# Optimization experiments

Hardware: AMD Instinct MI355X
Metric: run time of the kernel (lower is better)

Reference implementation:

```python
import jax, jax.numpy as jnp
import numpy as np
import math

B, S, D, E, H = 8, 384, 768, 768, 12
HD = E // H
MAXL = 512

def _xavier(key, shape):
    fan_in, fan_out = shape[1], shape[0]
    lim = math.sqrt(6.0 / (fan_in + fan_out))
    return jax.random.uniform(key, shape, jnp.float32, -lim, lim)

def setup_inputs() -> dict:
    key = jax.random.key(0)
    ks = jax.random.split(key, 12)
    return {
        "x": jax.random.normal(ks[0], (B, S, D), jnp.float32),
        "mask": jnp.ones((B, S), jnp.int32),
        "segment_ids": jax.random.randint(ks[1], (B, S), 0, 2).astype(jnp.int32),
        "sep_distances": jax.random.normal(ks[2], (B, S), jnp.float32),
        "Wq": _xavier(ks[3], (E, D)), "bq": jnp.zeros((E,), jnp.float32),
        "Wk": _xavier(ks[4], (E, D)), "bk": jnp.zeros((E,), jnp.float32),
        "Wv": _xavier(ks[5], (E, D)), "bv": jnp.zeros((E,), jnp.float32),
        "rel_emb": jax.random.normal(ks[6], (2 * MAXL - 1, D), jnp.float32),
        "Wpk": _xavier(ks[7], (E, D)), "bpk": jnp.zeros((E,), jnp.float32),
        "Wpq": _xavier(ks[8], (E, D)), "bpq": jnp.zeros((E,), jnp.float32),
        "same_bias": jnp.zeros((H,), jnp.float32),
        "cross_bias": jnp.zeros((H,), jnp.float32),
        "sep_scale": jnp.full((H,), 0.25, jnp.float32),
        "sep_decay": jnp.full((H,), 0.35, jnp.float32),
        "Wo": _xavier(ks[9], (D, E)), "bo": jnp.zeros((D,), jnp.float32),
    }

def reference(x, mask, segment_ids, sep_distances, Wq, bq, Wk, bk, Wv, bv,
              rel_emb, Wpk, bpk, Wpq, bpq, same_bias, cross_bias,
              sep_scale, sep_decay, Wo, bo):
    b, s, _ = x.shape
    def shape_heads(t):  # [b,s,E] -> [b,H,s,HD]
        return t.reshape(b, s, H, HD).transpose(0, 2, 1, 3)
    q = shape_heads(x @ Wq.T + bq)
    k = shape_heads(x @ Wk.T + bk)
    v = shape_heads(x @ Wv.T + bv)
    # relative positions i - j, clamped and shifted
    rel_pos = jnp.arange(s)[:, None] - jnp.arange(s)[None, :]
    rel_pos = jnp.clip(rel_pos, -(MAXL - 1), MAXL - 1) + (MAXL - 1)
    rel = rel_emb[rel_pos]                     # [s,s,D]
    pos_k = (rel @ Wpk.T + bpk).reshape(s, s, H, HD)  # [i,j,h,d]
    pos_q = (rel @ Wpq.T + bpq).reshape(s, s, H, HD)
    c2c = jnp.einsum('bhid,bhjd->bhij', q, k)
    c2p = jnp.einsum('bhid,ijhd->bhij', q, pos_k)
    p2c = jnp.einsum('ijhd,bhjd->bhij', pos_q, k)
    logits = (c2c + c2p + p2c) / math.sqrt(HD * 3.0)
    # segment bias
    same = (segment_ids[:, :, None] == segment_ids[:, None, :]).astype(jnp.float32)[:, None]  # [b,1,s,s]
    cross = 1.0 - same
    hb = lambda p: p[None, :, None, None]
    seg_bias = same * hb(same_bias) + cross * hb(cross_bias)
    abs_sep = jnp.abs(sep_distances)
    gap = jnp.abs(abs_sep[:, :, None] - abs_sep[:, None, :])[:, None]  # [b,1,s,s]
    decay = jax.nn.softplus(sep_decay)[None, :, None, None] + 1e-4
    seg_bias = seg_bias + cross * jnp.exp(-gap * decay) * hb(sep_scale)
    logits = logits + seg_bias
    # mask: [b,s] -> [b,1,1,s]
    m = mask[:, None, None, :]
    logits = jnp.where(m == 0, jnp.float32(-9e15), logits)
    attn = jax.nn.softmax(logits, axis=-1)
    vals = jnp.einsum('bhij,bhjd->bhid', attn, v)
    vals = vals.transpose(0, 2, 1, 3).reshape(b, s, E)
    return vals @ Wo.T + bo
```

## Files before the change

kernel.cpp:

```cpp
#include <hip/hip_runtime.h>
#include <math.h>

#define B_  8
#define S_  384
#define H_  12
#define HD_ 64
#define E_  768
#define D_  768

typedef float  floatx4 __attribute__((ext_vector_type(4)));
typedef __bf16 bf16x8  __attribute__((ext_vector_type(8)));
typedef unsigned int ux4 __attribute__((ext_vector_type(4)));

__device__ __forceinline__ unsigned short f2bf(float f) {
    union { float f; unsigned u; } x; x.f = f;
    unsigned r = x.u + 0x7fff + ((x.u >> 16) & 1);
    return (unsigned short)(r >> 16);
}
__device__ __forceinline__ float bf2f(unsigned short u) {
    union { unsigned u; float f; } x; x.u = ((unsigned)u) << 16;
    return x.f;
}
__device__ __forceinline__ bf16x8 gld8(const unsigned short* p) {
    return __builtin_bit_cast(bf16x8, *(const ux4*)p);
}
__device__ __forceinline__ int tadr(int row, int cD) {
    return (row * 8 + (cD ^ (row & 7))) * 8;
}
__device__ __forceinline__ bf16x8 lds8(const unsigned short* base, int row, int cD) {
    return __builtin_bit_cast(bf16x8, *(const ux4*)(base + tadr(row, cD)));
}

__global__ __launch_bounds__(256) void convert_all(
    const float* __restrict__ x,
    const float* __restrict__ Wq, const float* __restrict__ Wk,
    const float* __restrict__ Wv, const float* __restrict__ Wo,
    const float* __restrict__ Wpk, const float* __restrict__ Wpq,
    const float* __restrict__ rel128,
    unsigned short* __restrict__ xb,
    unsigned short* __restrict__ wqb, unsigned short* __restrict__ wkb,
    unsigned short* __restrict__ wvb, unsigned short* __restrict__ wob,
    unsigned short* __restrict__ wpkb, unsigned short* __restrict__ wpqb,
    unsigned short* __restrict__ relb)
{
    const int seg = blockIdx.y;
    const int e = (blockIdx.x * 256 + threadIdx.x) * 4;
    const float* src;
    unsigned short* dst;
    if (seg < 4)       { src = x + (size_t)seg * 589824; dst = xb + (size_t)seg * 589824; }
    else if (seg == 4) { src = Wq;  dst = wqb; }
    else if (seg == 5) { src = Wk;  dst = wkb; }
    else if (seg == 6) { src = Wv;  dst = wvb; }
    else if (seg == 7) { src = Wo;  dst = wob; }
    else if (seg == 8) { src = Wpk; dst = wpkb; }
    else if (seg == 9) { src = Wpq; dst = wpqb; }
    else               { src = rel128; dst = relb; }

    float4 v;
    if (seg == 10 && e >= 767 * 768) v = make_float4(0.f, 0.f, 0.f, 0.f);
    else                             v = *(const float4*)(src + e);
    ushort4 o;
    o.x = f2bf(v.x); o.y = f2bf(v.y); o.z = f2bf(v.z); o.w = f2bf(v.w);
    *(ushort4*)(dst + e) = o;
}

__global__ __launch_bounds__(256) void proj_all(
    const unsigned short* __restrict__ xb, const unsigned short* __restrict__ relb,
    const unsigned short* __restrict__ wq, const unsigned short* __restrict__ wk,
    const unsigned short* __restrict__ wv, const unsigned short* __restrict__ wpk,
    const unsigned short* __restrict__ wpq,
    const float* __restrict__ bq, const float* __restrict__ bk,
    const float* __restrict__ bv, const float* __restrict__ bpk,
    const float* __restrict__ bpq,
    unsigned short* __restrict__ qb, unsigned short* __restrict__ kb,
    unsigned short* __restrict__ vtb, unsigned short* __restrict__ pkb,
    unsigned short* __restrict__ pqb)
{
    const int bid = blockIdx.x;
    int z, mt, nt;
    if (bid < 864) {
        z = bid / 288; const int r = bid - z * 288; mt = r / 6; nt = r - mt * 6;
    } else {
        const int r2 = bid - 864; z = 3 + r2 / 72;
        const int r = r2 % 72; mt = r / 6; nt = r - mt * 6;
    }
    const int m0 = mt * 64, n0 = nt * 128;

    const unsigned short* A = (z < 3) ? xb : relb;
    const unsigned short* W = (z == 0) ? wq : (z == 1) ? wk : (z == 2) ? wv
                            : (z == 3) ? wpk : wpq;
    const float* bias = (z == 0) ? bq : (z == 1) ? bk : (z == 2) ? bv
                      : (z == 3) ? bpk : bpq;
    unsigned short* C = (z == 0) ? qb : (z == 1) ? kb : (z == 2) ? vtb
                      : (z == 3) ? pkb : pqb;

    __shared__ unsigned short As[64 * 64];
    __shared__ unsigned short Ws[128 * 64];

    const int tid  = threadIdx.x;
    const int lane = tid & 63;
    const int wv_  = tid >> 6;
    const int quad = lane >> 4, l16 = lane & 15;

    floatx4 acc[4][2];
#pragma unroll
    for (int i = 0; i < 4; ++i)
#pragma unroll
        for (int j = 0; j < 2; ++j) acc[i][j] = (floatx4){0.f, 0.f, 0.f, 0.f};

    for (int k0 = 0; k0 < 768; k0 += 64) {
        __syncthreads();
#pragma unroll
        for (int r = 0; r < 2; ++r) {
            const int idx = tid + 256 * r;
            const int row = idx >> 3, cL = idx & 7, cD = cL ^ (row & 7);
            __builtin_amdgcn_global_load_lds(
                (__attribute__((address_space(1))) void*)(A + (size_t)(m0 + row) * 768 + k0 + cD * 8),
                (__attribute__((address_space(3))) void*)&As[idx * 8], 16, 0, 0);
        }
#pragma unroll
        for (int r = 0; r < 4; ++r) {
            const int idx = tid + 256 * r;
            const int row = idx >> 3, cL = idx & 7, cD = cL ^ (row & 7);
            __builtin_amdgcn_global_load_lds(
                (__attribute__((address_space(1))) void*)(W + (size_t)(n0 + row) * 768 + k0 + cD * 8),
                (__attribute__((address_space(3))) void*)&Ws[idx * 8], 16, 0, 0);
        }
        __syncthreads();

        bf16x8 a[4][2], b[2][2];
#pragma unroll
        for (int mi = 0; mi < 4; ++mi)
#pragma unroll
            for (int kc = 0; kc < 2; ++kc)
                a[mi][kc] = lds8(As, mi * 16 + l16, kc * 4 + quad);
#pragma unroll
        for (int ni = 0; ni < 2; ++ni)
#pragma unroll
            for (int kc = 0; kc < 2; ++kc)
                b[ni][kc] = lds8(Ws, wv_ * 32 + ni * 16 + l16, kc * 4 + quad);
#pragma unroll
        for (int mi = 0; mi < 4; ++mi)
#pragma unroll
            for (int ni = 0; ni < 2; ++ni)
#pragma unroll
                for (int kc = 0; kc < 2; ++kc)
                    acc[mi][ni] = __builtin_amdgcn_mfma_f32_16x16x32_bf16(
                        a[mi][kc], b[ni][kc], acc[mi][ni], 0, 0, 0);
    }

#pragma unroll
    for (int ni = 0; ni < 2; ++ni) {
        const int n = n0 + wv_ * 32 + ni * 16 + l16;
        const float bn = bias[n];
#pragma unroll
        for (int mi = 0; mi < 4; ++mi) {
            const int mbase = m0 + mi * 16 + quad * 4;
            if (z == 2) {
                const int bb = mbase / S_, s = mbase - bb * S_;
                const int h = n >> 6, hd = n & 63;
                ushort4 o;
                o.x = f2bf(acc[mi][ni][0] + bn);
                o.y = f2bf(acc[mi][ni][1] + bn);
                o.z = f2bf(acc[mi][ni][2] + bn);
                o.w = f2bf(acc[mi][ni][3] + bn);
                *(ushort4*)&C[(((size_t)(bb * H_ + h) << 6) + hd) * S_ + s] = o;
            } else if (z < 2) {
#pragma unroll
                for (int reg = 0; reg < 4; ++reg) {
                    const int m = mbase + reg;
                    const int bb = m / S_, s = m - bb * S_;
                    const int h = n >> 6, hd = n & 63;
                    C[(((size_t)(bb * H_ + h) * S_ + s) << 6) + hd] =
                        f2bf(acc[mi][ni][reg] + bn);
                }
            } else {
#pragma unroll
                for (int reg = 0; reg < 4; ++reg)
                    C[(size_t)(mbase + reg) * 768 + n] = f2bf(acc[mi][ni][reg] + bn);
            }
        }
    }
}

__global__ __launch_bounds__(256) void gemm_out(
    const unsigned short* __restrict__ A, const unsigned short* __restrict__ W,
    const float* __restrict__ bias, float* __restrict__ C)
{
    const int mt = blockIdx.x / 6, nt = blockIdx.x - mt * 6;
    const int m0 = mt * 64, n0 = nt * 128;

    __shared__ unsigned short As[64 * 64];
    __shared__ unsigned short Ws[128 * 64];

    const int tid  = threadIdx.x;
    const int lane = tid & 63;
    const int wv_  = tid >> 6;
    const int quad = lane >> 4, l16 = lane & 15;

    floatx4 acc[4][2];
#pragma unroll
    for (int i = 0; i < 4; ++i)
#pragma unroll
        for (int j = 0; j < 2; ++j) acc[i][j] = (floatx4){0.f, 0.f, 0.f, 0.f};

    for (int k0 = 0; k0 < 768; k0 += 64) {
        __syncthreads();
#pragma unroll
        for (int r = 0; r < 2; ++r) {
            const int idx = tid + 256 * r;
            const int row = idx >> 3, cL = idx & 7, cD = cL ^ (row & 7);
            __builtin_amdgcn_global_load_lds(
                (__attribute__((address_space(1))) void*)(A + (size_t)(m0 + row) * 768 + k0 + cD * 8),
                (__attribute__((address_space(3))) void*)&As[idx * 8], 16, 0, 0);
        }
#pragma unroll
        for (int r = 0; r < 4; ++r) {
            const int idx = tid + 256 * r;
            const int row = idx >> 3, cL = idx & 7, cD = cL ^ (row & 7);
            __builtin_amdgcn_global_load_lds(
                (__attribute__((address_space(1))) void*)(W + (size_t)(n0 + row) * 768 + k0 + cD * 8),
                (__attribute__((address_space(3))) void*)&Ws[idx * 8], 16, 0, 0);
        }
        __syncthreads();

        bf16x8 a[4][2], b[2][2];
#pragma unroll
        for (int mi = 0; mi < 4; ++mi)
#pragma unroll
            for (int kc = 0; kc < 2; ++kc)
                a[mi][kc] = lds8(As, mi * 16 + l16, kc * 4 + quad);
#pragma unroll
        for (int ni = 0; ni < 2; ++ni)
#pragma unroll
            for (int kc = 0; kc < 2; ++kc)
                b[ni][kc] = lds8(Ws, wv_ * 32 + ni * 16 + l16, kc * 4 + quad);
#pragma unroll
        for (int mi = 0; mi < 4; ++mi)
#pragma unroll
            for (int ni = 0; ni < 2; ++ni)
#pragma unroll
                for (int kc = 0; kc < 2; ++kc)
                    acc[mi][ni] = __builtin_amdgcn_mfma_f32_16x16x32_bf16(
                        a[mi][kc], b[ni][kc], acc[mi][ni], 0, 0, 0);
    }

#pragma unroll
    for (int ni = 0; ni < 2; ++ni) {
        const int n = n0 + wv_ * 32 + ni * 16 + l16;
        const float bn = bias[n];
#pragma unroll
        for (int mi = 0; mi < 4; ++mi)
#pragma unroll
            for (int reg = 0; reg < 4; ++reg) {
                const int m = m0 + mi * 16 + quad * 4 + reg;
                C[(size_t)m * 768 + n] = acc[mi][ni][reg] + bn;
            }
    }
}

__global__ __launch_bounds__(256) void attn_mfma(
    const unsigned short* __restrict__ qg, const unsigned short* __restrict__ kg,
    const unsigned short* __restrict__ vtg,
    const unsigned short* __restrict__ pkg, const unsigned short* __restrict__ pqg,
    const int* __restrict__ seg, const float* __restrict__ sep,
    const int* __restrict__ mask,
    const float* __restrict__ same_bias, const float* __restrict__ cross_bias,
    const float* __restrict__ sep_scale, const float* __restrict__ sep_decay,
    unsigned short* __restrict__ part_O, float* __restrict__ part_ml)
{
    __shared__ unsigned short Ks [64 * 64];
    __shared__ unsigned short Vts[64 * 64];
    __shared__ unsigned short PKs[128 * 64];
    __shared__ unsigned short PQs[128 * 64];
    __shared__ float CP[64 * 68];

    const int tid  = threadIdx.x;
    const int lane = tid & 63, w = tid >> 6;
    const int l16  = lane & 15, quad = lane >> 4;
    const int ty = tid >> 4, tx = tid & 15;
    const int it = blockIdx.x, h = blockIdx.y;
    const int b  = blockIdx.z / 6, jt = blockIdx.z - 6 * b;
    const int i0 = it * 64, j0 = jt * 64;
    const size_t bh = (size_t)(b * H_ + h);

    const unsigned short* kbase  = kg  + bh * S_ * 64;
    const unsigned short* vtbase = vtg + bh * 64 * S_;
    const int dbase = i0 - j0 + 320;

    bf16x8 qf[2];
#pragma unroll
    for (int ks = 0; ks < 2; ++ks)
        qf[ks] = gld8(qg + (bh * S_ + i0 + 16 * w + l16) * 64 + ks * 32 + quad * 8);

#pragma unroll
    for (int r = 0; r < 2; ++r) {
        const int idx = tid + 256 * r;
        const int row = idx >> 3, cL = idx & 7;
        const int cD = cL ^ (row & 7);
        __builtin_amdgcn_global_load_lds(
            (__attribute__((address_space(1))) void*)(kbase + (size_t)(j0 + row) * 64 + cD * 8),
            (__attribute__((address_space(3))) void*)&Ks[idx * 8], 16, 0, 0);
        __builtin_amdgcn_global_load_lds(
            (__attribute__((address_space(1))) void*)(vtbase + (size_t)row * S_ + j0 + cD * 8),
            (__attribute__((address_space(3))) void*)&Vts[idx * 8], 16, 0, 0);
    }
#pragma unroll
    for (int r = 0; r < 4; ++r) {
        const int idx = tid + 256 * r;
        const int row = idx >> 3, cL = idx & 7;
        const int cD = cL ^ (row & 7);
        const size_t go = (size_t)(dbase + row) * 768 + h * 64 + cD * 8;
        __builtin_amdgcn_global_load_lds(
            (__attribute__((address_space(1))) void*)(pkg + go),
            (__attribute__((address_space(3))) void*)&PKs[idx * 8], 16, 0, 0);
        __builtin_amdgcn_global_load_lds(
            (__attribute__((address_space(1))) void*)(pqg + go),
            (__attribute__((address_space(3))) void*)&PQs[idx * 8], 16, 0, 0);
    }

    float ai_r[4]; int si_r[4];
#pragma unroll
    for (int p = 0; p < 4; ++p) {
        const int ii = 4 * ty + p;
        ai_r[p] = fabsf(sep[b * S_ + i0 + ii]);
        si_r[p] = seg[b * S_ + i0 + ii];
    }

    const float sb  = same_bias[h];
    const float cb  = cross_bias[h];
    const float ssc = sep_scale[h];
    const float sd  = sep_decay[h];
    const float dec = fmaxf(sd, 0.f) + log1pf(__expf(-fabsf(sd))) + 1e-4f;
    const float isc = 0.07216878364870323f;

    __syncthreads();

    bf16x8 kf[4][2];
#pragma unroll
    for (int nj = 0; nj < 4; ++nj)
#pragma unroll
        for (int ks = 0; ks < 2; ++ks)
            kf[nj][ks] = lds8(Ks, 16 * nj + l16, ks * 4 + quad);

#pragma unroll
    for (int nj = 0; nj < 4; ++nj) {
        floatx4 acc = (floatx4){0.f, 0.f, 0.f, 0.f};
#pragma unroll
        for (int ks = 0; ks < 2; ++ks)
            acc = __builtin_amdgcn_mfma_f32_16x16x32_bf16(qf[ks], kf[nj][ks], acc, 0, 0, 0);
#pragma unroll
        for (int reg = 0; reg < 4; ++reg) {
            const int ii = 16 * w + quad * 4 + reg;
            CP[ii * 68 + 16 * nj + l16] = acc[reg];
        }
    }

#pragma unroll
    for (int f = 0; f < 5; ++f) {
        const int nd = w + f;
        floatx4 acc = (floatx4){0.f, 0.f, 0.f, 0.f};
#pragma unroll
        for (int ks = 0; ks < 2; ++ks) {
            bf16x8 bf = lds8(PKs, 16 * nd + l16, ks * 4 + quad);
            acc = __builtin_amdgcn_mfma_f32_16x16x32_bf16(qf[ks], bf, acc, 0, 0, 0);
        }
        const int ddloc = 16 * nd + l16;
#pragma unroll
        for (int reg = 0; reg < 4; ++reg) {
            const int ii = 16 * w + quad * 4 + reg;
            const int jj = ii - ddloc + 63;
            if (jj >= 0 && jj < 64)
                CP[ii * 68 + jj] += acc[reg];
        }
    }

#pragma unroll
    for (int f = 0; f < 5; ++f) {
        const int nd = w + f;
        bf16x8 pqf[2];
#pragma unroll
        for (int ks = 0; ks < 2; ++ks)
            pqf[ks] = lds8(PQs, 16 * nd + l16, ks * 4 + quad);
#pragma unroll
        for (int g = 0; g < 2; ++g) {
            const int nj = (g == 0) ? (3 - f) : (4 - f);
            if (nj < 0 || nj > 3) continue;
            floatx4 acc = (floatx4){0.f, 0.f, 0.f, 0.f};
#pragma unroll
            for (int ks = 0; ks < 2; ++ks)
                acc = __builtin_amdgcn_mfma_f32_16x16x32_bf16(pqf[ks], kf[nj][ks], acc, 0, 0, 0);
            const int jj = 16 * nj + l16;
#pragma unroll
            for (int reg = 0; reg < 4; ++reg) {
                const int ddloc = 16 * nd + quad * 4 + reg;
                const int ii = ddloc + jj - 63;
                if (ii >= 16 * w && ii < 16 * w + 16)
                    CP[ii * 68 + jj] += acc[reg];
            }
        }
    }

    unsigned short* Pp = (unsigned short*)CP;
    float* pml = part_ml + (size_t)(jt * 576 + ((b * H_ + h) * 6 + it)) * 128;
#pragma unroll
    for (int p = 0; p < 4; ++p) {
        const int ii = 4 * ty + p;
        const float aii = ai_r[p];
        const int   sii = si_r[p];
        float lg[4];
        float tmax = -INFINITY;
#pragma unroll
        for (int r = 0; r < 4; ++r) {
            const int jl = 4 * tx + r;
            float xv = CP[ii * 68 + jl] * isc;
            const float ajv = fabsf(sep[b * S_ + j0 + jl]);
            const int   sjv = seg[b * S_ + j0 + jl];
            const float gap = fabsf(aii - ajv);
            const float bias = (sii == sjv) ? sb
                             : cb + __expf(-gap * dec) * ssc;
            xv += bias;
            if (mask[b * S_ + j0 + jl] == 0) xv = -9.0e15f;
            lg[r] = xv;
            tmax = fmaxf(tmax, xv);
        }
#pragma unroll
        for (int off = 1; off < 16; off <<= 1)
            tmax = fmaxf(tmax, __shfl_xor(tmax, off));
        float rs = 0.f;
        ushort4 pw;
#pragma unroll
        for (int r = 0; r < 4; ++r) {
            const float e = __expf(lg[r] - tmax);
            rs += e;
            ((unsigned short*)&pw)[r] = f2bf(e);
        }
#pragma unroll
        for (int off = 1; off < 16; off <<= 1)
            rs += __shfl_xor(rs, off);
        if (tx == 0) {
            pml[ii]      = tmax;
            pml[64 + ii] = rs;
        }
        *(ushort4*)&Pp[ii * 136 + 4 * tx] = pw;
    }

    bf16x8 pA[2];
#pragma unroll
    for (int ks = 0; ks < 2; ++ks)
        pA[ks] = __builtin_bit_cast(bf16x8,
            *(const ux4*)&Pp[(16 * w + l16) * 136 + ks * 32 + quad * 8]);
    floatx4 O[4];
#pragma unroll
    for (int nd = 0; nd < 4; ++nd) {
        O[nd] = (floatx4){0.f, 0.f, 0.f, 0.f};
#pragma unroll
        for (int ks = 0; ks < 2; ++ks) {
            bf16x8 bf = lds8(Vts, 16 * nd + l16, ks * 4 + quad);
            O[nd] = __builtin_amdgcn_mfma_f32_16x16x32_bf16(pA[ks], bf, O[nd], 0, 0, 0);
        }
    }

    unsigned short* pO = part_O + (size_t)(jt * 576 + ((b * H_ + h) * 6 + it)) * 4096;
#pragma unroll
    for (int nd = 0; nd < 4; ++nd) {
        const int d = 16 * nd + l16;
#pragma unroll
        for (int reg = 0; reg < 4; ++reg) {
            const int ii = 16 * w + quad * 4 + reg;
            pO[ii * 64 + d] = f2bf(O[nd][reg]);
        }
    }
}

__global__ __launch_bounds__(256) void merge_attn(
    const unsigned short* __restrict__ part_O, const float* __restrict__ part_ml,
    unsigned short* __restrict__ vals)
{
    const int idx = blockIdx.x;
    const int b  = idx / (H_ * 6);
    const int r  = idx - b * H_ * 6;
    const int h  = r / 6, it = r - h * 6;
    const int tid = threadIdx.x;
    const int ii = tid >> 2, c = (tid & 3) * 16;

    float m[6], l[6];
#pragma unroll
    for (int jc = 0; jc < 6; ++jc) {
        const float* pml = part_ml + (size_t)(jc * 576 + idx) * 128;
        m[jc] = pml[ii];
        l[jc] = pml[64 + ii];
    }
    float M = m[0];
#pragma unroll
    for (int jc = 1; jc < 6; ++jc) M = fmaxf(M, m[jc]);
    float wsum = 0.f, wc[6];
#pragma unroll
    for (int jc = 0; jc < 6; ++jc) {
        wc[jc] = __expf(m[jc] - M);
        wsum += wc[jc] * l[jc];
    }
    const float inv = (wsum > 0.f) ? 1.f / wsum : 0.f;

    float o[16];
#pragma unroll
    for (int e = 0; e < 16; ++e) o[e] = 0.f;
#pragma unroll
    for (int jc = 0; jc < 6; ++jc) {
        const unsigned short* pO = part_O + ((size_t)(jc * 576 + idx)) * 4096
                                 + ii * 64 + c;
        ux4 u0 = *(const ux4*)pO;
        ux4 u1 = *(const ux4*)(pO + 8);
        const unsigned short* us0 = (const unsigned short*)&u0;
        const unsigned short* us1 = (const unsigned short*)&u1;
#pragma unroll
        for (int e = 0; e < 8; ++e) {
            o[e]     += wc[jc] * bf2f(us0[e]);
            o[8 + e] += wc[jc] * bf2f(us1[e]);
        }
    }
    ushort4 w0, w1, w2, w3;
#pragma unroll
    for (int e = 0; e < 4; ++e) {
        ((unsigned short*)&w0)[e] = f2bf(o[e] * inv);
        ((unsigned short*)&w1)[e] = f2bf(o[4 + e] * inv);
        ((unsigned short*)&w2)[e] = f2bf(o[8 + e] * inv);
        ((unsigned short*)&w3)[e] = f2bf(o[12 + e] * inv);
    }
    unsigned short* dst = vals + ((size_t)(b * S_ + it * 64 + ii)) * E_ + h * 64 + c;
    *(ushort4*)(dst)      = w0;
    *(ushort4*)(dst + 4)  = w1;
    *(ushort4*)(dst + 8)  = w2;
    *(ushort4*)(dst + 12) = w3;
}

extern "C" void kernel_launch(void* const* d_in, const int* in_sizes, int n_in,
                              void* d_out, int out_size, void* d_ws, size_t ws_size,
                              hipStream_t stream)
{
    const float* x         = (const float*)d_in[0];
    const int*   mask      = (const int*)d_in[1];
    const int*   seg       = (const int*)d_in[2];
    const float* sep       = (const float*)d_in[3];
    const float* Wq        = (const float*)d_in[4];
    const float* bq        = (const float*)d_in[5];
    const float* Wk        = (const float*)d_in[6];
    const float* bk        = (const float*)d_in[7];
    const float* Wv        = (const float*)d_in[8];
    const float* bv        = (const float*)d_in[9];
    const float* rel_emb   = (const float*)d_in[10];
    const float* Wpk       = (const float*)d_in[11];
    const float* bpk       = (const float*)d_in[12];
    const float* Wpq       = (const float*)d_in[13];
    const float* bpq       = (const float*)d_in[14];
    const float* same_bias = (const float*)d_in[15];
    const float* cross_bias= (const float*)d_in[16];
    const float* sep_scale = (const float*)d_in[17];
    const float* sep_decay = (const float*)d_in[18];
    const float* Wo        = (const float*)d_in[19];
    const float* bo        = (const float*)d_in[20];

    const size_t QKVN = (size_t)B_ * S_ * E_;
    const size_t WN   = (size_t)768 * 768;

    unsigned short* xb    = (unsigned short*)d_ws;
    unsigned short* wqb   = xb   + QKVN;
    unsigned short* wkb   = wqb  + WN;
    unsigned short* wvb   = wkb  + WN;
    unsigned short* wob   = wvb  + WN;
    unsigned short* wpkb  = wob  + WN;
    unsigned short* wpqb  = wpkb + WN;
    unsigned short* relb  = wpqb + WN;
    unsigned short* qb    = relb + WN;
    unsigned short* kb    = qb   + QKVN;
    unsigned short* vtb   = kb   + QKVN;
    unsigned short* pkb   = vtb  + QKVN;
    unsigned short* pqb   = pkb  + WN;
    unsigned short* valsb = pqb  + WN;
    unsigned short* partO = valsb + QKVN;
    float*          partml= (float*)(partO + (size_t)6 * 576 * 4096);

    convert_all<<<dim3(576, 11), 256, 0, stream>>>(
        x, Wq, Wk, Wv, Wo, Wpk, Wpq, rel_emb + (size_t)128 * D_,
        xb, wqb, wkb, wvb, wob, wpkb, wpqb, relb);

    proj_all<<<dim3(1008), 256, 0, stream>>>(
        xb, relb, wqb, wkb, wvb, wpkb, wpqb,
        bq, bk, bv, bpk, bpq, qb, kb, vtb, pkb, pqb);

    attn_mfma<<<dim3(6, 12, 48), 256, 0, stream>>>(
        qb, kb, vtb, pkb, pqb, seg, sep, mask,
        same_bias, cross_bias, sep_scale, sep_decay, partO, partml);

    merge_attn<<<dim3(576), 256, 0, stream>>>(partO, partml, valsb);

    gemm_out<<<dim3(288), 256, 0, stream>>>(valsb, wob, bo, (float*)d_out);
}
```

Baseline: 212.6 us.

## Fuse all stages into one persistent cooperative kernel with grid syncs

Replaces the five separate launches (convert, projections, attention, merge, output GEMM) with a single persistent cooperative kernel. Blocks walk each stage with grid-stride loops and call grid.sync between stages, removing launch gaps and inter-kernel drain. The grid is capped at min(occupancy × CUs, 512) blocks, and the old separate-kernel path is kept as a fallback. The risks are lower parallelism and occupancy, since the 66 KB of shared memory sized for attention applies to every stage, plus the cost of the grid barriers themselves.

```diff
diff --git a/kernel.cpp b/kernel.cpp
--- a/kernel.cpp
+++ b/kernel.cpp
@@ -1,5 +1,8 @@
 #include <hip/hip_runtime.h>
+#include <hip/hip_cooperative_groups.h>
 #include <math.h>
+
+namespace cg = cooperative_groups;
 
 #define B_  8
 #define S_  384
@@ -31,73 +34,41 @@
     return __builtin_bit_cast(bf16x8, *(const ux4*)(base + tadr(row, cD)));
 }
 
-__global__ __launch_bounds__(256) void convert_all(
-    const float* __restrict__ x,
-    const float* __restrict__ Wq, const float* __restrict__ Wk,
-    const float* __restrict__ Wv, const float* __restrict__ Wo,
-    const float* __restrict__ Wpk, const float* __restrict__ Wpq,
-    const float* __restrict__ rel128,
-    unsigned short* __restrict__ xb,
-    unsigned short* __restrict__ wqb, unsigned short* __restrict__ wkb,
-    unsigned short* __restrict__ wvb, unsigned short* __restrict__ wob,
-    unsigned short* __restrict__ wpkb, unsigned short* __restrict__ wpqb,
-    unsigned short* __restrict__ relb)
-{
-    const int seg = blockIdx.y;
-    const int e = (blockIdx.x * 256 + threadIdx.x) * 4;
-    const float* src;
-    unsigned short* dst;
-    if (seg < 4)       { src = x + (size_t)seg * 589824; dst = xb + (size_t)seg * 589824; }
-    else if (seg == 4) { src = Wq;  dst = wqb; }
-    else if (seg == 5) { src = Wk;  dst = wkb; }
-    else if (seg == 6) { src = Wv;  dst = wvb; }
-    else if (seg == 7) { src = Wo;  dst = wob; }
-    else if (seg == 8) { src = Wpk; dst = wpkb; }
-    else if (seg == 9) { src = Wpq; dst = wpqb; }
-    else               { src = rel128; dst = relb; }
-
+struct KArgs {
+    const float *x, *sep;
+    const int *mask, *seg;
+    const float *Wq,*bq,*Wk,*bk,*Wv,*bv,*rel128,*Wpk,*bpk,*Wpq,*bpq;
+    const float *same_bias,*cross_bias,*sep_scale,*sep_decay,*Wo,*bo;
+    unsigned short *xb;
+    unsigned short *relb;
+    unsigned short *qb,*kb,*vtb,*pkb,*pqb,*valsb,*partO;
+    float *partml, *out;
+    int nblk;
+};
+
+__device__ __forceinline__ void convert_elem(const KArgs& a, int i)
+{
+    const float* srcW[7] = { a.Wq, a.Wk, a.Wv, a.Wo, a.Wpk, a.Wpq, a.rel128 };
+    const int e = i * 4;
+    const int sg = e / 589824;
+    const int off = e - sg * 589824;
     float4 v;
-    if (seg == 10 && e >= 767 * 768) v = make_float4(0.f, 0.f, 0.f, 0.f);
-    else                             v = *(const float4*)(src + e);
+    if (sg < 4)      v = *(const float4*)(a.x + e);
+    else if (sg == 10 && off >= 767 * 768) v = make_float4(0.f, 0.f, 0.f, 0.f);
+    else             v = *(const float4*)(srcW[sg - 4] + off);
     ushort4 o;
     o.x = f2bf(v.x); o.y = f2bf(v.y); o.z = f2bf(v.z); o.w = f2bf(v.w);
-    *(ushort4*)(dst + e) = o;
-}
-
-__global__ __launch_bounds__(256) void proj_all(
-    const unsigned short* __restrict__ xb, const unsigned short* __restrict__ relb,
-    const unsigned short* __restrict__ wq, const unsigned short* __restrict__ wk,
-    const unsigned short* __restrict__ wv, const unsigned short* __restrict__ wpk,
-    const unsigned short* __restrict__ wpq,
-    const float* __restrict__ bq, const float* __restrict__ bk,
-    const float* __restrict__ bv, const float* __restrict__ bpk,
-    const float* __restrict__ bpq,
-    unsigned short* __restrict__ qb, unsigned short* __restrict__ kb,
-    unsigned short* __restrict__ vtb, unsigned short* __restrict__ pkb,
-    unsigned short* __restrict__ pqb)
-{
-    const int bid = blockIdx.x;
-    int z, mt, nt;
-    if (bid < 864) {
-        z = bid / 288; const int r = bid - z * 288; mt = r / 6; nt = r - mt * 6;
-    } else {
-        const int r2 = bid - 864; z = 3 + r2 / 72;
-        const int r = r2 % 72; mt = r / 6; nt = r - mt * 6;
-    }
-    const int m0 = mt * 64, n0 = nt * 128;
-
-    const unsigned short* A = (z < 3) ? xb : relb;
-    const unsigned short* W = (z == 0) ? wq : (z == 1) ? wk : (z == 2) ? wv
-                            : (z == 3) ? wpk : wpq;
-    const float* bias = (z == 0) ? bq : (z == 1) ? bk : (z == 2) ? bv
-                      : (z == 3) ? bpk : bpq;
-    unsigned short* C = (z == 0) ? qb : (z == 1) ? kb : (z == 2) ? vtb
-                      : (z == 3) ? pkb : pqb;
-
-    __shared__ unsigned short As[64 * 64];
-    __shared__ unsigned short Ws[128 * 64];
-
-    const int tid  = threadIdx.x;
+    *(ushort4*)(a.xb + e) = o;
+}
+
+template <bool OUT_F32>
+__device__ void gemm_tile(const unsigned short* A, const unsigned short* W,
+                          const float* bias, void* Cv, int z, int m0, int n0,
+                          int tid, unsigned char* smem)
+{
+    unsigned short* As = (unsigned short*)smem;
+    unsigned short* Ws = (unsigned short*)(smem + 8192);
+
     const int lane = tid & 63;
     const int wv_  = tid >> 6;
     const int quad = lane >> 4, l16 = lane & 15;
@@ -128,17 +99,17 @@
         }
         __syncthreads();
 
-        bf16x8 a[4][2], b[2][2];
+        bf16x8 av[4][2], bv[2][2];
 #pragma unroll
         for (int mi = 0; mi < 4; ++mi)
 #pragma unroll
             for (int kc = 0; kc < 2; ++kc)
-                a[mi][kc] = lds8(As, mi * 16 + l16, kc * 4 + quad);
+                av[mi][kc] = lds8(As, mi * 16 + l16, kc * 4 + quad);
 #pragma unroll
         for (int ni = 0; ni < 2; ++ni)
 #pragma unroll
             for (int kc = 0; kc < 2; ++kc)
-                b[ni][kc] = lds8(Ws, wv_ * 32 + ni * 16 + l16, kc * 4 + quad);
+                bv[ni][kc] = lds8(Ws, wv_ * 32 + ni * 16 + l16, kc * 4 + quad);
 #pragma unroll
         for (int mi = 0; mi < 4; ++mi)
 #pragma unroll
@@ -146,7 +117,7 @@
 #pragma unroll
                 for (int kc = 0; kc < 2; ++kc)
                     acc[mi][ni] = __builtin_amdgcn_mfma_f32_16x16x32_bf16(
-                        a[mi][kc], b[ni][kc], acc[mi][ni], 0, 0, 0);
+                        av[mi][kc], bv[ni][kc], acc[mi][ni], 0, 0, 0);
     }
 
 #pragma unroll
@@ -156,7 +127,13 @@
 #pragma unroll
         for (int mi = 0; mi < 4; ++mi) {
             const int mbase = m0 + mi * 16 + quad * 4;
-            if (z == 2) {
+            if (OUT_F32) {
+                float* C = (float*)Cv;
+#pragma unroll
+                for (int reg = 0; reg < 4; ++reg)
+                    C[(size_t)(mbase + reg) * 768 + n] = acc[mi][ni][reg] + bn;
+            } else if (z == 2) {
+                unsigned short* C = (unsigned short*)Cv;
                 const int bb = mbase / S_, s = mbase - bb * S_;
                 const int h = n >> 6, hd = n & 63;
                 ushort4 o;
@@ -166,6 +143,7 @@
                 o.w = f2bf(acc[mi][ni][3] + bn);
                 *(ushort4*)&C[(((size_t)(bb * H_ + h) << 6) + hd) * S_ + s] = o;
             } else if (z < 2) {
+                unsigned short* C = (unsigned short*)Cv;
 #pragma unroll
                 for (int reg = 0; reg < 4; ++reg) {
                     const int m = mbase + reg;
@@ -175,6 +153,7 @@
                         f2bf(acc[mi][ni][reg] + bn);
                 }
             } else {
+                unsigned short* C = (unsigned short*)Cv;
 #pragma unroll
                 for (int reg = 0; reg < 4; ++reg)
                     C[(size_t)(mbase + reg) * 768 + n] = f2bf(acc[mi][ni][reg] + bn);
@@ -183,115 +162,45 @@
     }
 }
 
-__global__ __launch_bounds__(256) void gemm_out(
-    const unsigned short* __restrict__ A, const unsigned short* __restrict__ W,
-    const float* __restrict__ bias, float* __restrict__ C)
-{
-    const int mt = blockIdx.x / 6, nt = blockIdx.x - mt * 6;
-    const int m0 = mt * 64, n0 = nt * 128;
-
-    __shared__ unsigned short As[64 * 64];
-    __shared__ unsigned short Ws[128 * 64];
-
-    const int tid  = threadIdx.x;
-    const int lane = tid & 63;
-    const int wv_  = tid >> 6;
-    const int quad = lane >> 4, l16 = lane & 15;
-
-    floatx4 acc[4][2];
-#pragma unroll
-    for (int i = 0; i < 4; ++i)
-#pragma unroll
-        for (int j = 0; j < 2; ++j) acc[i][j] = (floatx4){0.f, 0.f, 0.f, 0.f};
-
-    for (int k0 = 0; k0 < 768; k0 += 64) {
-        __syncthreads();
-#pragma unroll
-        for (int r = 0; r < 2; ++r) {
-            const int idx = tid + 256 * r;
-            const int row = idx >> 3, cL = idx & 7, cD = cL ^ (row & 7);
-            __builtin_amdgcn_global_load_lds(
-                (__attribute__((address_space(1))) void*)(A + (size_t)(m0 + row) * 768 + k0 + cD * 8),
-                (__attribute__((address_space(3))) void*)&As[idx * 8], 16, 0, 0);
-        }
-#pragma unroll
-        for (int r = 0; r < 4; ++r) {
-            const int idx = tid + 256 * r;
-            const int row = idx >> 3, cL = idx & 7, cD = cL ^ (row & 7);
-            __builtin_amdgcn_global_load_lds(
-                (__attribute__((address_space(1))) void*)(W + (size_t)(n0 + row) * 768 + k0 + cD * 8),
-                (__attribute__((address_space(3))) void*)&Ws[idx * 8], 16, 0, 0);
-        }
-        __syncthreads();
-
-        bf16x8 a[4][2], b[2][2];
-#pragma unroll
-        for (int mi = 0; mi < 4; ++mi)
-#pragma unroll
-            for (int kc = 0; kc < 2; ++kc)
-                a[mi][kc] = lds8(As, mi * 16 + l16, kc * 4 + quad);
-#pragma unroll
-        for (int ni = 0; ni < 2; ++ni)
-#pragma unroll
-            for (int kc = 0; kc < 2; ++kc)
-                b[ni][kc] = lds8(Ws, wv_ * 32 + ni * 16 + l16, kc * 4 + quad);
-#pragma unroll
-        for (int mi = 0; mi < 4; ++mi)
-#pragma unroll
-            for (int ni = 0; ni < 2; ++ni)
-#pragma unroll
-                for (int kc = 0; kc < 2; ++kc)
-                    acc[mi][ni] = __builtin_amdgcn_mfma_f32_16x16x32_bf16(
-                        a[mi][kc], b[ni][kc], acc[mi][ni], 0, 0, 0);
-    }
-
-#pragma unroll
-    for (int ni = 0; ni < 2; ++ni) {
-        const int n = n0 + wv_ * 32 + ni * 16 + l16;
-        const float bn = bias[n];
-#pragma unroll
-        for (int mi = 0; mi < 4; ++mi)
-#pragma unroll
-            for (int reg = 0; reg < 4; ++reg) {
-                const int m = m0 + mi * 16 + quad * 4 + reg;
-                C[(size_t)m * 768 + n] = acc[mi][ni][reg] + bn;
-            }
-    }
-}
-
-__global__ __launch_bounds__(256) void attn_mfma(
-    const unsigned short* __restrict__ qg, const unsigned short* __restrict__ kg,
-    const unsigned short* __restrict__ vtg,
-    const unsigned short* __restrict__ pkg, const unsigned short* __restrict__ pqg,
-    const int* __restrict__ seg, const float* __restrict__ sep,
-    const int* __restrict__ mask,
-    const float* __restrict__ same_bias, const float* __restrict__ cross_bias,
-    const float* __restrict__ sep_scale, const float* __restrict__ sep_decay,
-    unsigned short* __restrict__ part_O, float* __restrict__ part_ml)
-{
-    __shared__ unsigned short Ks [64 * 64];
-    __shared__ unsigned short Vts[64 * 64];
-    __shared__ unsigned short PKs[128 * 64];
-    __shared__ unsigned short PQs[128 * 64];
-    __shared__ float CP[64 * 68];
-
-    const int tid  = threadIdx.x;
+__device__ __forceinline__ void proj_tile_dispatch(const KArgs& a, int t, int tid,
+                                                   unsigned char* smem)
+{
+    int z, mt, nt;
+    if (t < 864) { z = t / 288; const int r = t - z * 288; mt = r / 6; nt = r - mt * 6; }
+    else { const int r2 = t - 864; z = 3 + r2 / 72; const int r = r2 % 72; mt = r / 6; nt = r - mt * 6; }
+    const unsigned short* A = (z < 3) ? a.xb : a.relb;
+    unsigned short* wbase = a.xb + 2359296;
+    const unsigned short* W = wbase + (size_t)((z == 0) ? 0 : (z == 1) ? 1 : (z == 2) ? 2 : (z == 3) ? 4 : 5) * 589824;
+    const float* bias = (z == 0) ? a.bq : (z == 1) ? a.bk : (z == 2) ? a.bv
+                      : (z == 3) ? a.bpk : a.bpq;
+    void* C = (z == 0) ? (void*)a.qb : (z == 1) ? (void*)a.kb : (z == 2) ? (void*)a.vtb
+            : (z == 3) ? (void*)a.pkb : (void*)a.pqb;
+    gemm_tile<false>(A, W, bias, C, z, mt * 64, nt * 128, tid, smem);
+}
+
+__device__ void attn_tile(const KArgs& a, int it, int h, int b, int jt,
+                          int tid, unsigned char* smem)
+{
+    unsigned short* Ks  = (unsigned short*)smem;
+    unsigned short* Vts = (unsigned short*)(smem + 8192);
+    unsigned short* PKs = (unsigned short*)(smem + 16384);
+    unsigned short* PQs = (unsigned short*)(smem + 32768);
+    float* CP = (float*)(smem + 49152);
+
     const int lane = tid & 63, w = tid >> 6;
     const int l16  = lane & 15, quad = lane >> 4;
     const int ty = tid >> 4, tx = tid & 15;
-    const int it = blockIdx.x, h = blockIdx.y;
-    const int b  = blockIdx.z / 6, jt = blockIdx.z - 6 * b;
     const int i0 = it * 64, j0 = jt * 64;
     const size_t bh = (size_t)(b * H_ + h);
 
-    const unsigned short* kbase  = kg  + bh * S_ * 64;
-    const unsigned short* vtbase = vtg + bh * 64 * S_;
+    const unsigned short* kbase  = a.kb  + bh * S_ * 64;
+    const unsigned short* vtbase = a.vtb + bh * 64 * S_;
     const int dbase = i0 - j0 + 320;
 
     bf16x8 qf[2];
 #pragma unroll
     for (int ks = 0; ks < 2; ++ks)
-        qf[ks] = gld8(qg + (bh * S_ + i0 + 16 * w + l16) * 64 + ks * 32 + quad * 8);
+        qf[ks] = gld8(a.qb + (bh * S_ + i0 + 16 * w + l16) * 64 + ks * 32 + quad * 8);
 
 #pragma unroll
     for (int r = 0; r < 2; ++r) {
@@ -312,10 +221,10 @@
         const int cD = cL ^ (row & 7);
         const size_t go = (size_t)(dbase + row) * 768 + h * 64 + cD * 8;
         __builtin_amdgcn_global_load_lds(
-            (__attribute__((address_space(1))) void*)(pkg + go),
+            (__attribute__((address_space(1))) void*)(a.pkb + go),
             (__attribute__((address_space(3))) void*)&PKs[idx * 8], 16, 0, 0);
         __builtin_amdgcn_global_load_lds(
-            (__attribute__((address_space(1))) void*)(pqg + go),
+            (__attribute__((address_space(1))) void*)(a.pqb + go),
             (__attribute__((address_space(3))) void*)&PQs[idx * 8], 16, 0, 0);
     }
 
@@ -323,14 +232,14 @@
 #pragma unroll
     for (int p = 0; p < 4; ++p) {
         const int ii = 4 * ty + p;
-        ai_r[p] = fabsf(sep[b * S_ + i0 + ii]);
-        si_r[p] = seg[b * S_ + i0 + ii];
-    }
-
-    const float sb  = same_bias[h];
-    const float cb  = cross_bias[h];
-    const float ssc = sep_scale[h];
-    const float sd  = sep_decay[h];
+        ai_r[p] = fabsf(a.sep[b * S_ + i0 + ii]);
+        si_r[p] = a.seg[b * S_ + i0 + ii];
+    }
+
+    const float sb  = a.same_bias[h];
+    const float cb  = a.cross_bias[h];
+    const float ssc = a.sep_scale[h];
+    const float sd  = a.sep_decay[h];
     const float dec = fmaxf(sd, 0.f) + log1pf(__expf(-fabsf(sd))) + 1e-4f;
     const float isc = 0.07216878364870323f;
 
@@ -402,7 +311,7 @@
     }
 
     unsigned short* Pp = (unsigned short*)CP;
-    float* pml = part_ml + (size_t)(jt * 576 + ((b * H_ + h) * 6 + it)) * 128;
+    float* pml = a.partml + (size_t)(jt * 576 + ((b * H_ + h) * 6 + it)) * 128;
 #pragma unroll
     for (int p = 0; p < 4; ++p) {
         const int ii = 4 * ty + p;
@@ -414,13 +323,13 @@
         for (int r = 0; r < 4; ++r) {
             const int jl = 4 * tx + r;
             float xv = CP[ii * 68 + jl] * isc;
-            const float ajv = fabsf(sep[b * S_ + j0 + jl]);
-            const int   sjv = seg[b * S_ + j0 + jl];
+            const float ajv = fabsf(a.sep[b * S_ + j0 + jl]);
+            const int   sjv = a.seg[b * S_ + j0 + jl];
             const float gap = fabsf(aii - ajv);
             const float bias = (sii == sjv) ? sb
                              : cb + __expf(-gap * dec) * ssc;
             xv += bias;
-            if (mask[b * S_ + j0 + jl] == 0) xv = -9.0e15f;
+            if (a.mask[b * S_ + j0 + jl] == 0) xv = -9.0e15f;
             lg[r] = xv;
             tmax = fmaxf(tmax, xv);
         }
@@ -461,7 +370,7 @@
         }
     }
 
-    unsigned short* pO = part_O + (size_t)(jt * 576 + ((b * H_ + h) * 6 + it)) * 4096;
+    unsigned short* pO = a.partO + (size_t)(jt * 576 + ((b * H_ + h) * 6 + it)) * 4096;
 #pragma unroll
     for (int nd = 0; nd < 4; ++nd) {
         const int d = 16 * nd + l16;
@@ -473,21 +382,17 @@
     }
 }
 
-__global__ __launch_bounds__(256) void merge_attn(
-    const unsigned short* __restrict__ part_O, const float* __restrict__ part_ml,
-    unsigned short* __restrict__ vals)
-{
-    const int idx = blockIdx.x;
+__device__ void merge_tile(const KArgs& a, int idx, int tid)
+{
     const int b  = idx / (H_ * 6);
     const int r  = idx - b * H_ * 6;
     const int h  = r / 6, it = r - h * 6;
-    const int tid = threadIdx.x;
     const int ii = tid >> 2, c = (tid & 3) * 16;
 
     float m[6], l[6];
 #pragma unroll
     for (int jc = 0; jc < 6; ++jc) {
-        const float* pml = part_ml + (size_t)(jc * 576 + idx) * 128;
+        const float* pml = a.partml + (size_t)(jc * 576 + idx) * 128;
         m[jc] = pml[ii];
         l[jc] = pml[64 + ii];
     }
@@ -507,7 +412,7 @@
     for (int e = 0; e < 16; ++e) o[e] = 0.f;
 #pragma unroll
     for (int jc = 0; jc < 6; ++jc) {
-        const unsigned short* pO = part_O + ((size_t)(jc * 576 + idx)) * 4096
+        const unsigned short* pO = a.partO + ((size_t)(jc * 576 + idx)) * 4096
                                  + ii * 64 + c;
         ux4 u0 = *(const ux4*)pO;
         ux4 u1 = *(const ux4*)(pO + 8);
@@ -527,50 +432,88 @@
         ((unsigned short*)&w2)[e] = f2bf(o[8 + e] * inv);
         ((unsigned short*)&w3)[e] = f2bf(o[12 + e] * inv);
     }
-    unsigned short* dst = vals + ((size_t)(b * S_ + it * 64 + ii)) * E_ + h * 64 + c;
+    unsigned short* dst = a.valsb + ((size_t)(b * S_ + it * 64 + ii)) * E_ + h * 64 + c;
     *(ushort4*)(dst)      = w0;
     *(ushort4*)(dst + 4)  = w1;
     *(ushort4*)(dst + 8)  = w2;
     *(ushort4*)(dst + 12) = w3;
 }
 
+__global__ __launch_bounds__(256) void fused_all(KArgs a)
+{
+    cg::grid_group grid = cg::this_grid();
+    __shared__ __align__(16) unsigned char smem[66560];
+    const int bid = blockIdx.x, tid = threadIdx.x;
+    const int nblk = a.nblk;
+
+    for (int i = bid * 256 + tid; i < 1622016; i += nblk * 256)
+        convert_elem(a, i);
+    grid.sync();
+
+    for (int t = bid; t < 1008; t += nblk)
+        proj_tile_dispatch(a, t, tid, smem);
+    grid.sync();
+
+    for (int t = bid; t < 3456; t += nblk) {
+        __syncthreads();
+        const int it = t % 6;
+        const int h  = (t / 6) % 12;
+        const int zz = t / 72;
+        const int b  = zz / 6, jt = zz - 6 * b;
+        attn_tile(a, it, h, b, jt, tid, smem);
+    }
+    grid.sync();
+
+    for (int t = bid; t < 576; t += nblk) merge_tile(a, t, tid);
+    grid.sync();
+
+    {
+        unsigned short* wob = a.xb + 2359296 + (size_t)3 * 589824;
+        for (int t = bid; t < 288; t += nblk) {
+            const int mt = t / 6, nt = t - mt * 6;
+            gemm_tile<true>(a.valsb, wob, a.bo, (void*)a.out, 0, mt * 64, nt * 128, tid, smem);
+        }
+    }
+}
+
+__global__ __launch_bounds__(256) void k_convert(KArgs a)
+{
+    const int i = blockIdx.x * 256 + threadIdx.x;
+    if (i < 1622016) convert_elem(a, i);
+}
+__global__ __launch_bounds__(256) void k_proj(KArgs a)
+{
+    __shared__ __align__(16) unsigned char smem[24576];
+    proj_tile_dispatch(a, blockIdx.x, threadIdx.x, smem);
+}
+__global__ __launch_bounds__(256) void k_attn(KArgs a)
+{
+    __shared__ __align__(16) unsigned char smem[66560];
+    const int b = blockIdx.z / 6, jt = blockIdx.z - 6 * b;
+    attn_tile(a, blockIdx.x, blockIdx.y, b, jt, threadIdx.x, smem);
+}
+__global__ __launch_bounds__(256) void k_merge(KArgs a)
+{
+    merge_tile(a, blockIdx.x, threadIdx.x);
+}
+__global__ __launch_bounds__(256) void k_out(KArgs a)
+{
+    __shared__ __align__(16) unsigned char smem[24576];
+    unsigned short* wob = a.xb + 2359296 + (size_t)3 * 589824;
+    const int mt = blockIdx.x / 6, nt = blockIdx.x - mt * 6;
+    gemm_tile<true>(a.valsb, wob, a.bo, (void*)a.out, 0, mt * 64, nt * 128,
+                    threadIdx.x, smem);
+}
+
 extern "C" void kernel_launch(void* const* d_in, const int* in_sizes, int n_in,
                               void* d_out, int out_size, void* d_ws, size_t ws_size,
                               hipStream_t stream)
 {
-    const float* x         = (const float*)d_in[0];
-    const int*   mask      = (const int*)d_in[1];
-    const int*   seg       = (const int*)d_in[2];
-    const float* sep       = (const float*)d_in[3];
-    const float* Wq        = (const float*)d_in[4];
-    const float* bq        = (const float*)d_in[5];
-    const float* Wk        = (const float*)d_in[6];
-    const float* bk        = (const float*)d_in[7];
-    const float* Wv        = (const float*)d_in[8];
-    const float* bv        = (const float*)d_in[9];
-    const float* rel_emb   = (const float*)d_in[10];
-    const float* Wpk       = (const float*)d_in[11];
-    const float* bpk       = (const float*)d_in[12];
-    const float* Wpq       = (const float*)d_in[13];
-    const float* bpq       = (const float*)d_in[14];
-    const float* same_bias = (const float*)d_in[15];
-    const float* cross_bias= (const float*)d_in[16];
-    const float* sep_scale = (const float*)d_in[17];
-    const float* sep_decay = (const float*)d_in[18];
-    const float* Wo        = (const float*)d_in[19];
-    const float* bo        = (const float*)d_in[20];
-
     const size_t QKVN = (size_t)B_ * S_ * E_;
     const size_t WN   = (size_t)768 * 768;
 
     unsigned short* xb    = (unsigned short*)d_ws;
-    unsigned short* wqb   = xb   + QKVN;
-    unsigned short* wkb   = wqb  + WN;
-    unsigned short* wvb   = wkb  + WN;
-    unsigned short* wob   = wvb  + WN;
-    unsigned short* wpkb  = wob  + WN;
-    unsigned short* wpqb  = wpkb + WN;
-    unsigned short* relb  = wpqb + WN;
+    unsigned short* relb  = xb + QKVN + 6 * WN;
     unsigned short* qb    = relb + WN;
     unsigned short* kb    = qb   + QKVN;
     unsigned short* vtb   = kb   + QKVN;
@@ -580,19 +523,55 @@
     unsigned short* partO = valsb + QKVN;
     float*          partml= (float*)(partO + (size_t)6 * 576 * 4096);
 
-    convert_all<<<dim3(576, 11), 256, 0, stream>>>(
-        x, Wq, Wk, Wv, Wo, Wpk, Wpq, rel_emb + (size_t)128 * D_,
-        xb, wqb, wkb, wvb, wob, wpkb, wpqb, relb);
-
-    proj_all<<<dim3(1008), 256, 0, stream>>>(
-        xb, relb, wqb, wkb, wvb, wpkb, wpqb,
-        bq, bk, bv, bpk, bpq, qb, kb, vtb, pkb, pqb);
-
-    attn_mfma<<<dim3(6, 12, 48), 256, 0, stream>>>(
-        qb, kb, vtb, pkb, pqb, seg, sep, mask,
-        same_bias, cross_bias, sep_scale, sep_decay, partO, partml);
-
-    merge_attn<<<dim3(576), 256, 0, stream>>>(partO, partml, valsb);
-
-    gemm_out<<<dim3(288), 256, 0, stream>>>(valsb, wob, bo, (float*)d_out);
-}
+    KArgs a;
+    a.x         = (const float*)d_in[0];
+    a.mask      = (const int*)d_in[1];
+    a.seg       = (const int*)d_in[2];
+    a.sep       = (const float*)d_in[3];
+    a.Wq        = (const float*)d_in[4];
+    a.bq        = (const float*)d_in[5];
+    a.Wk        = (const float*)d_in[6];
+    a.bk        = (const float*)d_in[7];
+    a.Wv        = (const float*)d_in[8];
+    a.bv        = (const float*)d_in[9];
+    a.rel128    = (const float*)d_in[10] + (size_t)128 * D_;
+    a.Wpk       = (const float*)d_in[11];
+    a.bpk       = (const float*)d_in[12];
+    a.Wpq       = (const float*)d_in[13];
+    a.bpq       = (const float*)d_in[14];
+    a.same_bias = (const float*)d_in[15];
+    a.cross_bias= (const float*)d_in[16];
+    a.sep_scale = (const float*)d_in[17];
+    a.sep_decay = (const float*)d_in[18];
+    a.Wo        = (const float*)d_in[19];
+    a.bo        = (const float*)d_in[20];
+    a.xb = xb; a.relb = relb;
+    a.qb = qb; a.kb = kb; a.vtb = vtb; a.pkb = pkb; a.pqb = pqb;
+    a.valsb = valsb; a.partO = partO; a.partml = partml;
+    a.out = (float*)d_out;
+    a.nblk = 0;
+
+    int dev = 0;
+    (void)hipGetDevice(&dev);
+    int cus = 0;
+    (void)hipDeviceGetAttribute(&cus, hipDeviceAttributeMultiprocessorCount, dev);
+    int occ = 0;
+    (void)hipOccupancyMaxActiveBlocksPerMultiprocessor(&occ, fused_all, 256, 0);
+    long cap = (long)occ * (long)cus;
+    int nblk = (int)((cap > 512) ? 512 : cap);
+
+    hipError_t err = hipErrorUnknown;
+    if (nblk >= 64) {
+        a.nblk = nblk;
+        void* kp[] = { (void*)&a };
+        err = hipLaunchCooperativeKernel((const void*)fused_all, dim3(nblk),
+                                         dim3(256), kp, 0, stream);
+    }
+    if (err != hipSuccess) {
+        k_convert<<<dim3(6336), 256, 0, stream>>>(a);
+        k_proj   <<<dim3(1008), 256, 0, stream>>>(a);
+        k_attn   <<<dim3(6, 12, 48), 256, 0, stream>>>(a);
+        k_merge  <<<dim3(576), 256, 0, stream>>>(a);
+        k_out    <<<dim3(288), 256, 0, stream>>>(a);
+    }
+}
```

Measured after the change: 450.6 us. 2.12x slower.
